# Kernel tuning notes

Measured on AMD Instinct MI355X. Metric: run time of the kernel, lower is better.

The kernel has to match this reference:

```python
import jax, jax.numpy as jnp
import numpy as np

N_NODES = 50000
D_FEAT = 128
N_EDGES = 600000
HIDDEN = 256


def setup_inputs() -> dict:
    key = jax.random.key(0)
    k1, k2, k3, k4 = jax.random.split(key, 4)
    nodes = jax.random.normal(k1, (N_NODES, D_FEAT), dtype=jnp.float32)
    senders = jax.random.randint(k2, (N_EDGES,), 0, N_NODES, dtype=jnp.int32)
    receivers = jax.random.randint(k3, (N_EDGES,), 0, N_NODES, dtype=jnp.int32)
    # Dense(hidden): input dim = 2*D_FEAT (concat of aggregated + self features)
    W = jax.random.normal(k4, (2 * D_FEAT, HIDDEN), dtype=jnp.float32) / np.sqrt(2 * D_FEAT)
    b = jnp.zeros((HIDDEN,), dtype=jnp.float32)
    return {"nodes": nodes, "senders": senders, "receivers": receivers, "W": W, "b": b}


def reference(nodes, senders, receivers, W, b):
    n = nodes.shape[0]
    # segment_mean: gather sender features, scatter-sum onto receivers, divide by counts
    gathered = nodes[senders]                                    # [E, D]
    sums = jax.ops.segment_sum(gathered, receivers, num_segments=n)  # [N, D]
    counts = jax.ops.segment_sum(
        jnp.ones((senders.shape[0],), dtype=nodes.dtype), receivers, num_segments=n
    )                                                            # [N]
    h_e = sums / jnp.maximum(counts, 1.0)[:, None]               # mean (0 for empty segments)
    h = jnp.concatenate([h_e, nodes], axis=-1)                   # [N, 2D]
    out = jax.nn.relu(h @ W + b)                                 # [N, HIDDEN]
    return out
```

## Files before the change

kernel.cpp:

```cpp
#include <hip/hip_runtime.h>
#include <hip/hip_bf16.h>

#define N_NODES 50000
#define D_FEAT  128
#define N_EDGES 600000
#define HIDDEN  256
#define K_DIM   256

#define BUCKET   64
#define ZERO_ROW 50000
#define M_TILE   32
#define NTILES   1563
#define NPAD     (NTILES * M_TILE)
#define H_STRIDE 264

typedef __attribute__((ext_vector_type(8))) short bf16x8;
typedef __attribute__((ext_vector_type(4))) float f32x4;

__device__ __forceinline__ unsigned short f32_to_bf16(float f) {
    unsigned int u = __float_as_uint(f);
    unsigned int r = (u + 0x7fffu + ((u >> 16) & 1u)) >> 16;
    return (unsigned short)r;
}
__device__ __forceinline__ unsigned int pack_bf16x2(float lo, float hi) {
    return (unsigned int)f32_to_bf16(lo) | ((unsigned int)f32_to_bf16(hi) << 16);
}
__device__ __forceinline__ float bf_lo(unsigned int v) {
    return __uint_as_float(v << 16);
}
__device__ __forceinline__ float bf_hi(unsigned int v) {
    return __uint_as_float(v & 0xffff0000u);
}

__global__ __launch_bounds__(256) void build_conv_repack(
    const int* __restrict__ senders,
    const int* __restrict__ receivers,
    const float* __restrict__ nodes,
    const float* __restrict__ W,
    unsigned short* __restrict__ edges16,
    unsigned int* __restrict__ cnt,
    unsigned int* __restrict__ nb,
    unsigned short* __restrict__ Wp) {
    const int gid = blockIdx.x * 256 + threadIdx.x;
    const int gsz = gridDim.x * 256;
    for (int e = gid; e < N_EDGES; e += gsz) {
        int r = receivers[e];
        unsigned int slot = atomicAdd(&cnt[r], 1u);
        if (slot < (unsigned int)BUCKET)
            edges16[(size_t)r * BUCKET + slot] = (unsigned short)senders[e];
    }
    for (int p = gid; p < N_NODES * 64; p += gsz) {
        const float2 v = *(const float2*)(nodes + (size_t)p * 2);
        nb[p] = pack_bf16x2(v.x, v.y);
    }
    if (gid < 64) nb[(size_t)ZERO_ROW * 64 + gid] = 0u;
    for (int t = gid; t < 65536; t += gsz) {
        int kt = t >> 13;
        int n  = (t >> 5) & 255;
        int q  = (t >> 3) & 3;
        int j  = t & 7;
        int k  = kt * 32 + q * 8 + j;
        Wp[t] = f32_to_bf16(W[k * 256 + n]);
    }
}

__global__ __launch_bounds__(256) void gather_mean_gemm(
    const unsigned int* __restrict__ nb,
    const unsigned int* __restrict__ cnt,
    const unsigned short* __restrict__ edges16,
    const unsigned short* __restrict__ Wp,
    const float* __restrict__ bias,
    float* __restrict__ out) {
    __shared__ __align__(16) unsigned int h32[M_TILE * (H_STRIDE / 2)];

    const int m0   = blockIdx.x * M_TILE;
    const int tid  = threadIdx.x;
    const int wave = tid >> 6;
    const int lane = tid & 63;

    unsigned int cc[8];
    #pragma unroll
    for (int i = 0; i < 8; i++) {
        int m = m0 + wave * 8 + i;
        unsigned int c = (m < N_NODES) ? cnt[m] : 0u;
        cc[i] = c < (unsigned int)BUCKET ? c : (unsigned int)BUCKET;
    }

    #pragma unroll
    for (int ip = 0; ip < 4; ip++) {
        const int rA = wave * 8 + ip * 2;
        const int rB = rA + 1;
        const unsigned int* epA =
            (const unsigned int*)(edges16 + (size_t)(m0 + rA) * BUCKET);
        const unsigned int* epB =
            (const unsigned int*)(edges16 + (size_t)(m0 + rB) * BUCKET);

        unsigned int wA[8], wB[8];
        #pragma unroll
        for (int j = 0; j < 8; j++) { wA[j] = epA[j]; wB[j] = epB[j]; }

        unsigned int vA[16], vB[16];
        #pragma unroll
        for (int j = 0; j < 8; j++) {
            vA[2*j]   = nb[(size_t)(wA[j] & 0xffffu) * 64 + lane];
            vA[2*j+1] = nb[(size_t)(wA[j] >> 16)     * 64 + lane];
            vB[2*j]   = nb[(size_t)(wB[j] & 0xffffu) * 64 + lane];
            vB[2*j+1] = nb[(size_t)(wB[j] >> 16)     * 64 + lane];
        }
        unsigned int selfA = nb[(size_t)(m0 + rA) * 64 + lane];
        unsigned int selfB = nb[(size_t)(m0 + rB) * 64 + lane];

        float a0 = 0.f, a1 = 0.f, a2 = 0.f, a3 = 0.f;
        float b0 = 0.f, b1 = 0.f, b2 = 0.f, b3 = 0.f;
        #pragma unroll
        for (int j = 0; j < 16; j += 2) {
            a0 += bf_lo(vA[j]);   a1 += bf_hi(vA[j]);
            a2 += bf_lo(vA[j+1]); a3 += bf_hi(vA[j+1]);
            b0 += bf_lo(vB[j]);   b1 += bf_hi(vB[j]);
            b2 += bf_lo(vB[j+1]); b3 += bf_hi(vB[j+1]);
        }

        unsigned int cA = cc[ip * 2], cB = cc[ip * 2 + 1];
        if (cA > 16u) {
            unsigned int cp = (cA + 15u) & ~15u;
            for (unsigned int s = 16; s < cp; s += 16) {
                unsigned int w[8], v[16];
                #pragma unroll
                for (int j = 0; j < 8; j++) w[j] = epA[(s >> 1) + j];
                #pragma unroll
                for (int j = 0; j < 8; j++) {
                    v[2*j]   = nb[(size_t)(w[j] & 0xffffu) * 64 + lane];
                    v[2*j+1] = nb[(size_t)(w[j] >> 16)     * 64 + lane];
                }
                #pragma unroll
                for (int j = 0; j < 16; j += 2) {
                    a0 += bf_lo(v[j]);   a1 += bf_hi(v[j]);
                    a2 += bf_lo(v[j+1]); a3 += bf_hi(v[j+1]);
                }
            }
        }
        if (cB > 16u) {
            unsigned int cp = (cB + 15u) & ~15u;
            for (unsigned int s = 16; s < cp; s += 16) {
                unsigned int w[8], v[16];
                #pragma unroll
                for (int j = 0; j < 8; j++) w[j] = epB[(s >> 1) + j];
                #pragma unroll
                for (int j = 0; j < 8; j++) {
                    v[2*j]   = nb[(size_t)(w[j] & 0xffffu) * 64 + lane];
                    v[2*j+1] = nb[(size_t)(w[j] >> 16)     * 64 + lane];
                }
                #pragma unroll
                for (int j = 0; j < 16; j += 2) {
                    b0 += bf_lo(v[j]);   b1 += bf_hi(v[j]);
                    b2 += bf_lo(v[j+1]); b3 += bf_hi(v[j+1]);
                }
            }
        }

        float invA = 1.0f / fmaxf((float)cA, 1.0f);
        float invB = 1.0f / fmaxf((float)cB, 1.0f);
        h32[rA * (H_STRIDE / 2) + lane]      = pack_bf16x2((a0 + a2) * invA,
                                                           (a1 + a3) * invA);
        h32[rA * (H_STRIDE / 2) + 64 + lane] = selfA;
        h32[rB * (H_STRIDE / 2) + lane]      = pack_bf16x2((b0 + b2) * invB,
                                                           (b1 + b3) * invB);
        h32[rB * (H_STRIDE / 2) + 64 + lane] = selfB;
    }
    __syncthreads();

    const unsigned short* h = (const unsigned short*)h32;
    const int nbase = wave * 64;
    const int rsel  = lane & 15;
    const int quad  = lane >> 4;

    f32x4 acc[2][4] = {};

    for (int kk = 0; kk < K_DIM; kk += 32) {
        bf16x8 a[2], bw[4];
        #pragma unroll
        for (int mt = 0; mt < 2; mt++) {
            const unsigned short* pa =
                &h[(mt * 16 + rsel) * H_STRIDE + kk + quad * 8];
            a[mt] = *(const bf16x8*)pa;
        }
        int kt = kk >> 5;
        #pragma unroll
        for (int nt = 0; nt < 4; nt++) {
            int n = nbase + nt * 16 + rsel;
            bw[nt] = *(const bf16x8*)&Wp[kt * 8192 + n * 32 + quad * 8];
        }
        #pragma unroll
        for (int mt = 0; mt < 2; mt++)
            #pragma unroll
            for (int nt = 0; nt < 4; nt++)
                acc[mt][nt] = __builtin_amdgcn_mfma_f32_16x16x32_bf16(
                    a[mt], bw[nt], acc[mt][nt], 0, 0, 0);
    }

    #pragma unroll
    for (int nt = 0; nt < 4; nt++) {
        int n = nbase + nt * 16 + rsel;
        float bn = bias[n];
        #pragma unroll
        for (int mt = 0; mt < 2; mt++) {
            #pragma unroll
            for (int r = 0; r < 4; r++) {
                int m = m0 + mt * 16 + quad * 4 + r;
                if (m < N_NODES) {
                    float v = acc[mt][nt][r] + bn;
                    out[(size_t)m * HIDDEN + n] = fmaxf(v, 0.0f);
                }
            }
        }
    }
}

extern "C" void kernel_launch(void* const* d_in, const int* in_sizes, int n_in,
                              void* d_out, int out_size, void* d_ws, size_t ws_size,
                              hipStream_t stream) {
    const float* nodes     = (const float*)d_in[0];
    const int*   senders   = (const int*)d_in[1];
    const int*   receivers = (const int*)d_in[2];
    const float* W         = (const float*)d_in[3];
    const float* bias      = (const float*)d_in[4];
    float*       out       = (float*)d_out;

    unsigned short* edges16 = (unsigned short*)d_ws;
    unsigned int*   cnt     = (unsigned int*)(edges16 + (size_t)NPAD * BUCKET);
    unsigned int*   nb      = cnt + N_NODES;
    unsigned short* Wp      = (unsigned short*)(nb + (size_t)(N_NODES + 1) * 64);

    hipMemsetD16Async((hipDeviceptr_t)edges16, 0xC350,
                      (size_t)NPAD * BUCKET, stream);
    hipMemsetAsync(cnt, 0, (size_t)N_NODES * sizeof(unsigned int), stream);

    build_conv_repack<<<dim3(1024), dim3(256), 0, stream>>>(
        senders, receivers, nodes, W, edges16, cnt, nb, Wp);

    gather_mean_gemm<<<dim3(NTILES), dim3(256), 0, stream>>>(
        nb, cnt, edges16, Wp, bias, out);
}
```

Before: 185.2 us.

## Shift zero row to index 0, merge memsets, gather four rows per batch

Moves the zero padding row to the front of the packed node table and stores sender indices offset by one. The edge buckets can then be cleared together with the counters in one zero memset instead of a 16-bit fill plus a separate memset. The gather loop now handles four receiver rows at a time instead of two, so more independent global loads are in flight per wave. The cost is higher register pressure, which may lower occupancy. The self-feature read for out-of-range padding rows is also redirected to the zero row.

```diff
diff --git a/kernel.cpp b/kernel.cpp
--- a/kernel.cpp
+++ b/kernel.cpp
@@ -8,11 +8,11 @@
 #define K_DIM   256
 
 #define BUCKET   64
-#define ZERO_ROW 50000
 #define M_TILE   32
 #define NTILES   1563
 #define NPAD     (NTILES * M_TILE)
 #define H_STRIDE 264
+
 
 typedef __attribute__((ext_vector_type(8))) short bf16x8;
 typedef __attribute__((ext_vector_type(4))) float f32x4;
@@ -47,13 +47,14 @@
         int r = receivers[e];
         unsigned int slot = atomicAdd(&cnt[r], 1u);
         if (slot < (unsigned int)BUCKET)
-            edges16[(size_t)r * BUCKET + slot] = (unsigned short)senders[e];
+            edges16[(size_t)r * BUCKET + slot] =
+                (unsigned short)(senders[e] + 1);
     }
     for (int p = gid; p < N_NODES * 64; p += gsz) {
         const float2 v = *(const float2*)(nodes + (size_t)p * 2);
-        nb[p] = pack_bf16x2(v.x, v.y);
-    }
-    if (gid < 64) nb[(size_t)ZERO_ROW * 64 + gid] = 0u;
+        nb[64 + p] = pack_bf16x2(v.x, v.y);
+    }
+    if (gid < 64) nb[gid] = 0u;
     for (int t = gid; t < 65536; t += gsz) {
         int kt = t >> 13;
         int n  = (t >> 5) & 255;
@@ -87,85 +88,76 @@
     }
 
     #pragma unroll
-    for (int ip = 0; ip < 4; ip++) {
-        const int rA = wave * 8 + ip * 2;
-        const int rB = rA + 1;
-        const unsigned int* epA =
-            (const unsigned int*)(edges16 + (size_t)(m0 + rA) * BUCKET);
-        const unsigned int* epB =
-            (const unsigned int*)(edges16 + (size_t)(m0 + rB) * BUCKET);
-
-        unsigned int wA[8], wB[8];
-        #pragma unroll
-        for (int j = 0; j < 8; j++) { wA[j] = epA[j]; wB[j] = epB[j]; }
-
-        unsigned int vA[16], vB[16];
-        #pragma unroll
-        for (int j = 0; j < 8; j++) {
-            vA[2*j]   = nb[(size_t)(wA[j] & 0xffffu) * 64 + lane];
-            vA[2*j+1] = nb[(size_t)(wA[j] >> 16)     * 64 + lane];
-            vB[2*j]   = nb[(size_t)(wB[j] & 0xffffu) * 64 + lane];
-            vB[2*j+1] = nb[(size_t)(wB[j] >> 16)     * 64 + lane];
-        }
-        unsigned int selfA = nb[(size_t)(m0 + rA) * 64 + lane];
-        unsigned int selfB = nb[(size_t)(m0 + rB) * 64 + lane];
-
-        float a0 = 0.f, a1 = 0.f, a2 = 0.f, a3 = 0.f;
-        float b0 = 0.f, b1 = 0.f, b2 = 0.f, b3 = 0.f;
-        #pragma unroll
-        for (int j = 0; j < 16; j += 2) {
-            a0 += bf_lo(vA[j]);   a1 += bf_hi(vA[j]);
-            a2 += bf_lo(vA[j+1]); a3 += bf_hi(vA[j+1]);
-            b0 += bf_lo(vB[j]);   b1 += bf_hi(vB[j]);
-            b2 += bf_lo(vB[j+1]); b3 += bf_hi(vB[j+1]);
-        }
-
-        unsigned int cA = cc[ip * 2], cB = cc[ip * 2 + 1];
-        if (cA > 16u) {
-            unsigned int cp = (cA + 15u) & ~15u;
-            for (unsigned int s = 16; s < cp; s += 16) {
-                unsigned int w[8], v[16];
-                #pragma unroll
-                for (int j = 0; j < 8; j++) w[j] = epA[(s >> 1) + j];
-                #pragma unroll
-                for (int j = 0; j < 8; j++) {
-                    v[2*j]   = nb[(size_t)(w[j] & 0xffffu) * 64 + lane];
-                    v[2*j+1] = nb[(size_t)(w[j] >> 16)     * 64 + lane];
+    for (int ig = 0; ig < 2; ig++) {
+        const int rbase = wave * 8 + ig * 4;
+
+        unsigned int w[4][8];
+        #pragma unroll
+        for (int r = 0; r < 4; r++) {
+            const unsigned int* ep = (const unsigned int*)
+                (edges16 + (size_t)(m0 + rbase + r) * BUCKET);
+            #pragma unroll
+            for (int j = 0; j < 8; j++) w[r][j] = ep[j];
+        }
+
+        unsigned int v[4][16], selfp[4];
+        #pragma unroll
+        for (int r = 0; r < 4; r++) {
+            #pragma unroll
+            for (int j = 0; j < 8; j++) {
+                v[r][2*j]   = nb[(size_t)(w[r][j] & 0xffffu) * 64 + lane];
+                v[r][2*j+1] = nb[(size_t)(w[r][j] >> 16)     * 64 + lane];
+            }
+            int m = m0 + rbase + r;
+            int ms = (m < N_NODES) ? (m + 1) : 0;
+            selfp[r] = nb[(size_t)ms * 64 + lane];
+        }
+
+        float a[4][4];
+        #pragma unroll
+        for (int r = 0; r < 4; r++) {
+            a[r][0] = a[r][1] = a[r][2] = a[r][3] = 0.f;
+            #pragma unroll
+            for (int j = 0; j < 16; j += 2) {
+                a[r][0] += bf_lo(v[r][j]);   a[r][1] += bf_hi(v[r][j]);
+                a[r][2] += bf_lo(v[r][j+1]); a[r][3] += bf_hi(v[r][j+1]);
+            }
+        }
+
+        #pragma unroll
+        for (int r = 0; r < 4; r++) {
+            unsigned int c = cc[ig * 4 + r];
+            if (c > 16u) {
+                const unsigned int* ep = (const unsigned int*)
+                    (edges16 + (size_t)(m0 + rbase + r) * BUCKET);
+                unsigned int cp = (c + 15u) & ~15u;
+                for (unsigned int s = 16; s < cp; s += 16) {
+                    unsigned int ww[8], vv[16];
+                    #pragma unroll
+                    for (int j = 0; j < 8; j++) ww[j] = ep[(s >> 1) + j];
+                    #pragma unroll
+                    for (int j = 0; j < 8; j++) {
+                        vv[2*j]   = nb[(size_t)(ww[j] & 0xffffu) * 64 + lane];
+                        vv[2*j+1] = nb[(size_t)(ww[j] >> 16)     * 64 + lane];
+                    }
+                    #pragma unroll
+                    for (int j = 0; j < 16; j += 2) {
+                        a[r][0] += bf_lo(vv[j]);   a[r][1] += bf_hi(vv[j]);
+                        a[r][2] += bf_lo(vv[j+1]); a[r][3] += bf_hi(vv[j+1]);
+                    }
                 }
-                #pragma unroll
-                for (int j = 0; j < 16; j += 2) {
-                    a0 += bf_lo(v[j]);   a1 += bf_hi(v[j]);
-                    a2 += bf_lo(v[j+1]); a3 += bf_hi(v[j+1]);
-                }
-            }
-        }
-        if (cB > 16u) {
-            unsigned int cp = (cB + 15u) & ~15u;
-            for (unsigned int s = 16; s < cp; s += 16) {
-                unsigned int w[8], v[16];
-                #pragma unroll
-                for (int j = 0; j < 8; j++) w[j] = epB[(s >> 1) + j];
-                #pragma unroll
-                for (int j = 0; j < 8; j++) {
-                    v[2*j]   = nb[(size_t)(w[j] & 0xffffu) * 64 + lane];
-                    v[2*j+1] = nb[(size_t)(w[j] >> 16)     * 64 + lane];
-                }
-                #pragma unroll
-                for (int j = 0; j < 16; j += 2) {
-                    b0 += bf_lo(v[j]);   b1 += bf_hi(v[j]);
-                    b2 += bf_lo(v[j+1]); b3 += bf_hi(v[j+1]);
-                }
-            }
-        }
-
-        float invA = 1.0f / fmaxf((float)cA, 1.0f);
-        float invB = 1.0f / fmaxf((float)cB, 1.0f);
-        h32[rA * (H_STRIDE / 2) + lane]      = pack_bf16x2((a0 + a2) * invA,
-                                                           (a1 + a3) * invA);
-        h32[rA * (H_STRIDE / 2) + 64 + lane] = selfA;
-        h32[rB * (H_STRIDE / 2) + lane]      = pack_bf16x2((b0 + b2) * invB,
-                                                           (b1 + b3) * invB);
-        h32[rB * (H_STRIDE / 2) + 64 + lane] = selfB;
+            }
+        }
+
+        #pragma unroll
+        for (int r = 0; r < 4; r++) {
+            float inv = 1.0f / fmaxf((float)cc[ig * 4 + r], 1.0f);
+            int row = rbase + r;
+            h32[row * (H_STRIDE / 2) + lane] =
+                pack_bf16x2((a[r][0] + a[r][2]) * inv,
+                            (a[r][1] + a[r][3]) * inv);
+            h32[row * (H_STRIDE / 2) + 64 + lane] = selfp[r];
+        }
     }
     __syncthreads();
 
@@ -231,9 +223,10 @@
     unsigned int*   nb      = cnt + N_NODES;
     unsigned short* Wp      = (unsigned short*)(nb + (size_t)(N_NODES + 1) * 64);
 
-    hipMemsetD16Async((hipDeviceptr_t)edges16, 0xC350,
-                      (size_t)NPAD * BUCKET, stream);
-    hipMemsetAsync(cnt, 0, (size_t)N_NODES * sizeof(unsigned int), stream);
+    hipMemsetAsync(d_ws, 0,
+                   (size_t)NPAD * BUCKET * sizeof(unsigned short) +
+                   (size_t)N_NODES * sizeof(unsigned int),
+                   stream);
 
     build_conv_repack<<<dim3(1024), dim3(256), 0, stream>>>(
         senders, receivers, nodes, W, edges16, cnt, nb, Wp);
```

Result: no change. 186.7 us (+0.8%).
